# Kernel tuning notes

Measured on AMD Instinct MI355X. Metric: run time of the kernel, lower is better.

## Reference

```python
import jax, jax.numpy as jnp
import numpy as np

N = 50000
E = 800000
IN_CH = 512
OUT_CH = 64
ITERATIONS = 3  # adjacency power order; iterations-1 spmm steps


def setup_inputs() -> dict:
    key = jax.random.key(0)
    k1, k2, k3, k4, k5 = jax.random.split(key, 5)
    adj_indices = jax.random.randint(k1, (2, E), 0, N, dtype=jnp.int32)
    adj_values = jax.random.uniform(k2, (E,), dtype=jnp.float32)
    features = jax.random.normal(k3, (N, IN_CH), dtype=jnp.float32)
    # xavier-uniform init bounds
    bw = float(np.sqrt(6.0 / (IN_CH + OUT_CH)))
    weight = jax.random.uniform(k4, (IN_CH, OUT_CH), minval=-bw, maxval=bw, dtype=jnp.float32)
    bb = float(np.sqrt(6.0 / (1 + OUT_CH)))
    bias = jax.random.uniform(k5, (1, OUT_CH), minval=-bb, maxval=bb, dtype=jnp.float32)
    return {"adj_indices": adj_indices, "adj_values": adj_values,
            "features": features, "weight": weight, "bias": bias}


def reference(adj_indices, adj_values, features, weight, bias):
    # dense projection: [N, in] @ [in, out] -> [N, out]
    x = features @ weight
    # dropout is identity in eval mode (training=False)
    row, col = adj_indices[0], adj_indices[1]
    # (iterations - 1) sparse-dense matmuls: x <- A @ x
    for _ in range(ITERATIONS - 1):
        gathered = adj_values[:, None] * x[col]          # [E, out]
        x = jax.ops.segment_sum(gathered, row, num_segments=N)
    return x + bias
```

## Files before the change

### kernel.cpp

```cpp
#include <hip/hip_runtime.h>
#include <hip/hip_bf16.h>
#include <hip/hip_fp16.h>

#define NN 50000
#define INCH 512
#define OUTCH 64
#define NTILES 3125
#define MAXD 48
#define GB 782
#define SB 512

typedef __attribute__((ext_vector_type(8))) short short8;
typedef __attribute__((ext_vector_type(4))) float floatx4;

__device__ __forceinline__ unsigned packbf2(float a, float b) {
    __hip_bfloat162 h = __float22bfloat162_rn(make_float2(a, b));
    unsigned r;
    __builtin_memcpy(&r, &h, 4);
    return r;
}
__device__ __forceinline__ unsigned short f2bf(float f) {
    unsigned u = __float_as_uint(f);
    return (unsigned short)((u + 0x7FFFu + ((u >> 16) & 1u)) >> 16);
}
__device__ __forceinline__ float bf2f(unsigned short u) {
    return __uint_as_float(((unsigned)u) << 16);
}

__global__ __launch_bounds__(256) void prep_kernel(const float* __restrict__ W,
                                                   unsigned short* __restrict__ Wbf,
                                                   int* __restrict__ deg) {
    const int i = blockIdx.x * 256 + threadIdx.x;
    if (i < NN / 4)
        *reinterpret_cast<uint4*>(deg + i * 4) = uint4{0u, 0u, 0u, 0u};
    if (i < INCH * OUTCH) {
        const int k = i >> 6;
        const int n = i & 63;
        Wbf[n * INCH + k] = f2bf(W[i]);
    }
}

__global__ __launch_bounds__(256, 4) void fused_gemm_scatter(
        const float* __restrict__ A, const unsigned short* __restrict__ Wbf,
        unsigned short* __restrict__ C,
        const int* __restrict__ rows, const int* __restrict__ cols,
        const float* __restrict__ vals, int* __restrict__ deg,
        unsigned* __restrict__ ell, int E_) {
    __shared__ unsigned short ldsT[4][16 * 64];
    const int t = threadIdx.x;

    if (blockIdx.x >= GB) {
        for (int e = (blockIdx.x - GB) * 256 + t; e < E_; e += SB * 256) {
            const int r = __builtin_nontemporal_load(rows + e);
            const int c = __builtin_nontemporal_load(cols + e);
            const float v = __builtin_nontemporal_load(vals + e);
            const int slot = atomicAdd(&deg[r], 1);
            const unsigned short hv = __half_as_ushort(__float2half(v));
            if (slot < MAXD)
                ell[(size_t)r * MAXD + slot] = (unsigned)c | ((unsigned)hv << 16);
        }
        return;
    }

    const int lane = t & 63;
    const int wave = t >> 6;
    const int tile = blockIdx.x * 4 + wave;
    if (tile >= NTILES) return;
    const int rbase = tile * 16;
    const int frow = lane & 15;
    const int quad = lane >> 4;
    const float* Ap = A + (size_t)(rbase + frow) * INCH + quad * 8;
    const unsigned short* Bp = Wbf + frow * INCH + quad * 8;

    floatx4 acc[4] = {floatx4{0,0,0,0}, floatx4{0,0,0,0}, floatx4{0,0,0,0}, floatx4{0,0,0,0}};

#pragma unroll
    for (int c = 0; c < 16; ++c) {
        const floatx4 a0 = __builtin_nontemporal_load((const floatx4*)(Ap + c * 32));
        const floatx4 a1 = __builtin_nontemporal_load((const floatx4*)(Ap + c * 32 + 4));
        short8 bfr[4];
#pragma unroll
        for (int f = 0; f < 4; ++f)
            bfr[f] = *(const short8*)(Bp + (size_t)f * 16 * INCH + c * 32);
        uint4 au;
        au.x = packbf2(a0[0], a0[1]);
        au.y = packbf2(a0[2], a0[3]);
        au.z = packbf2(a1[0], a1[1]);
        au.w = packbf2(a1[2], a1[3]);
        const short8 af = *(const short8*)&au;
#pragma unroll
        for (int f = 0; f < 4; ++f)
            acc[f] = __builtin_amdgcn_mfma_f32_16x16x32_bf16(af, bfr[f], acc[f], 0, 0, 0);
    }

    unsigned short* myT = ldsT[wave];
#pragma unroll
    for (int f = 0; f < 4; ++f)
#pragma unroll
        for (int reg = 0; reg < 4; ++reg)
            myT[(quad * 4 + reg) * 64 + f * 16 + frow] = f2bf(acc[f][reg]);
    unsigned short* Cw = C + (size_t)rbase * OUTCH;
#pragma unroll
    for (int it = 0; it < 2; ++it) {
        const short8 v = *(const short8*)&myT[it * 512 + lane * 8];
        __builtin_nontemporal_store(v, (short8*)(Cw + it * 512 + lane * 8));
    }
}

template <bool LAST>
__global__ __launch_bounds__(256) void spmm_ell(const int* __restrict__ deg,
                                                const unsigned* __restrict__ ell,
                                                const unsigned short* __restrict__ xin,
                                                void* __restrict__ xout_,
                                                const float* __restrict__ bias) {
    const int b = blockIdx.x;
    const int xcd = b & 7;
    const int half = xcd >> 2;
    const int rowgrp = (b >> 3) * 4 + (xcd & 3);
    const int t = threadIdx.x;
    const int lane = t & 63;
    const int eslot = lane >> 2;
    const int cg = lane & 3;
    const int row = rowgrp * 4 + (t >> 6);
    int d = __builtin_nontemporal_load(deg + row);
    d = d < MAXD ? d : MAXD;
    const unsigned* ebase = ell + (size_t)row * MAXD;

    unsigned p0 = __builtin_nontemporal_load(ebase + eslot);
    unsigned p1 = __builtin_nontemporal_load(ebase + eslot + 16);
    unsigned p2 = __builtin_nontemporal_load(ebase + eslot + 32);
    if (eslot >= d)      p0 = 0u;
    if (eslot + 16 >= d) p1 = 0u;
    if (eslot + 32 >= d) p2 = 0u;

    const unsigned short* xh = xin + half * 32 + cg * 8;
    float acc[8] = {0.f, 0.f, 0.f, 0.f, 0.f, 0.f, 0.f, 0.f};

    auto gath = [&](unsigned P) {
        const short8 xv = *(const short8*)(xh + (size_t)(P & 0xFFFFu) * OUTCH);
        const float v = __half2float(__ushort_as_half((unsigned short)(P >> 16)));
#pragma unroll
        for (int j = 0; j < 8; ++j)
            acc[j] = fmaf(v, bf2f((unsigned short)xv[j]), acc[j]);
    };
    if (d > 0)  gath(p0);
    if (d > 16) gath(p1);
    if (d > 32) gath(p2);

#pragma unroll
    for (int j = 0; j < 8; ++j) {
        acc[j] += __shfl_xor(acc[j], 4, 64);
        acc[j] += __shfl_xor(acc[j], 8, 64);
        acc[j] += __shfl_xor(acc[j], 16, 64);
        acc[j] += __shfl_xor(acc[j], 32, 64);
    }

    if (eslot == 0) {
        const int chb = half * 32 + cg * 8;
        if (LAST) {
            float* op = (float*)xout_ + (size_t)row * OUTCH + chb;
            const floatx4 b0 = *(const floatx4*)(bias + chb);
            const floatx4 b1 = *(const floatx4*)(bias + chb + 4);
            floatx4 o0, o1;
            o0[0] = acc[0] + b0[0]; o0[1] = acc[1] + b0[1];
            o0[2] = acc[2] + b0[2]; o0[3] = acc[3] + b0[3];
            o1[0] = acc[4] + b1[0]; o1[1] = acc[5] + b1[1];
            o1[2] = acc[6] + b1[2]; o1[3] = acc[7] + b1[3];
            __builtin_nontemporal_store(o0, (floatx4*)op);
            __builtin_nontemporal_store(o1, (floatx4*)(op + 4));
        } else {
            unsigned short* op = (unsigned short*)xout_ + (size_t)row * OUTCH + chb;
            short8 o;
#pragma unroll
            for (int j = 0; j < 8; ++j) o[j] = (short)f2bf(acc[j]);
            __builtin_nontemporal_store(o, (short8*)op);
        }
    }
}

extern "C" void kernel_launch(void* const* d_in, const int* in_sizes, int n_in,
                              void* d_out, int out_size, void* d_ws, size_t ws_size,
                              hipStream_t stream) {
    const int*   adj   = (const int*)d_in[0];
    const float* avals = (const float*)d_in[1];
    const float* feat  = (const float*)d_in[2];
    const float* W     = (const float*)d_in[3];
    const float* bias  = (const float*)d_in[4];
    float* out = (float*)d_out;

    const int E_ = in_sizes[1];
    const int* rows = adj;
    const int* cols = adj + E_;

    unsigned short* x0  = (unsigned short*)d_ws;
    unsigned short* x1  = x0 + (size_t)NN * OUTCH;
    unsigned short* Wbf = x1 + (size_t)NN * OUTCH;
    unsigned* ell = (unsigned*)(Wbf + (size_t)OUTCH * INCH);
    int* deg = (int*)(ell + (size_t)NN * MAXD);

    prep_kernel<<<128, 256, 0, stream>>>(W, Wbf, deg);

    fused_gemm_scatter<<<GB + SB, 256, 0, stream>>>(feat, Wbf, x0, rows, cols, avals,
                                                    deg, ell, E_);

    spmm_ell<false><<<25000, 256, 0, stream>>>(deg, ell, x0, x1, nullptr);
    spmm_ell<true><<<25000, 256, 0, stream>>>(deg, ell, x1, out, bias);
}
```

Before: 288.9 us.

## Split scatter into row-range passes and SpMM into per-half-channel launches

Separates the fused GEMM+scatter kernel into a standalone GEMM and four scatter passes, each handling a quarter of the destination rows, so atomics and ELL writes hit a smaller working set that fits in cache. The SpMM is split into two launches per iteration, each covering 32 channels, which replaces the XCD-aware block swizzle. Intermediate stores become regular rather than nontemporal so x1 stays cached for the next step. The cost is re-reading the row array four times, losing the overlap between GEMM and scatter, and more kernel launches.

```diff
diff --git a/kernel.cpp b/kernel.cpp
--- a/kernel.cpp
+++ b/kernel.cpp
@@ -8,7 +8,8 @@
 #define NTILES 3125
 #define MAXD 48
 #define GB 782
-#define SB 512
+#define SCB 512
+#define ROWS_PER_PASS 12500
 
 typedef __attribute__((ext_vector_type(8))) short short8;
 typedef __attribute__((ext_vector_type(4))) float floatx4;
@@ -40,28 +41,11 @@
     }
 }
 
-__global__ __launch_bounds__(256, 4) void fused_gemm_scatter(
+__global__ __launch_bounds__(256, 4) void gemm_kernel(
         const float* __restrict__ A, const unsigned short* __restrict__ Wbf,
-        unsigned short* __restrict__ C,
-        const int* __restrict__ rows, const int* __restrict__ cols,
-        const float* __restrict__ vals, int* __restrict__ deg,
-        unsigned* __restrict__ ell, int E_) {
+        unsigned short* __restrict__ C) {
     __shared__ unsigned short ldsT[4][16 * 64];
     const int t = threadIdx.x;
-
-    if (blockIdx.x >= GB) {
-        for (int e = (blockIdx.x - GB) * 256 + t; e < E_; e += SB * 256) {
-            const int r = __builtin_nontemporal_load(rows + e);
-            const int c = __builtin_nontemporal_load(cols + e);
-            const float v = __builtin_nontemporal_load(vals + e);
-            const int slot = atomicAdd(&deg[r], 1);
-            const unsigned short hv = __half_as_ushort(__float2half(v));
-            if (slot < MAXD)
-                ell[(size_t)r * MAXD + slot] = (unsigned)c | ((unsigned)hv << 16);
-        }
-        return;
-    }
-
     const int lane = t & 63;
     const int wave = t >> 6;
     const int tile = blockIdx.x * 4 + wave;
@@ -107,22 +91,37 @@
     }
 }
 
+__global__ __launch_bounds__(256) void scatter_pass(
+        const int* __restrict__ rows, const int* __restrict__ cols,
+        const float* __restrict__ vals, int* __restrict__ deg,
+        unsigned* __restrict__ ell, int E_, int rowlo) {
+    for (int e = blockIdx.x * 256 + threadIdx.x; e < E_; e += SCB * 256) {
+        const int r = __builtin_nontemporal_load(rows + e);
+        if ((unsigned)(r - rowlo) < (unsigned)ROWS_PER_PASS) {
+            const int c = __builtin_nontemporal_load(cols + e);
+            const float v = __builtin_nontemporal_load(vals + e);
+            const int slot = atomicAdd(&deg[r], 1);
+            if (slot < MAXD) {
+                const unsigned short hv = __half_as_ushort(__float2half(v));
+                ell[(size_t)r * MAXD + slot] = (unsigned)c | ((unsigned)hv << 16);
+            }
+        }
+    }
+}
+
 template <bool LAST>
-__global__ __launch_bounds__(256) void spmm_ell(const int* __restrict__ deg,
-                                                const unsigned* __restrict__ ell,
-                                                const unsigned short* __restrict__ xin,
-                                                void* __restrict__ xout_,
-                                                const float* __restrict__ bias) {
-    const int b = blockIdx.x;
-    const int xcd = b & 7;
-    const int half = xcd >> 2;
-    const int rowgrp = (b >> 3) * 4 + (xcd & 3);
+__global__ __launch_bounds__(256) void spmm_half(const int* __restrict__ deg,
+                                                 const unsigned* __restrict__ ell,
+                                                 const unsigned short* __restrict__ xin,
+                                                 void* __restrict__ xout_,
+                                                 const float* __restrict__ bias,
+                                                 int chbase) {
     const int t = threadIdx.x;
     const int lane = t & 63;
     const int eslot = lane >> 2;
     const int cg = lane & 3;
-    const int row = rowgrp * 4 + (t >> 6);
-    int d = __builtin_nontemporal_load(deg + row);
+    const int row = blockIdx.x * 4 + (t >> 6);
+    int d = deg[row];
     d = d < MAXD ? d : MAXD;
     const unsigned* ebase = ell + (size_t)row * MAXD;
 
@@ -133,7 +132,7 @@
     if (eslot + 16 >= d) p1 = 0u;
     if (eslot + 32 >= d) p2 = 0u;
 
-    const unsigned short* xh = xin + half * 32 + cg * 8;
+    const unsigned short* xh = xin + chbase + cg * 8;
     float acc[8] = {0.f, 0.f, 0.f, 0.f, 0.f, 0.f, 0.f, 0.f};
 
     auto gath = [&](unsigned P) {
@@ -156,7 +155,7 @@
     }
 
     if (eslot == 0) {
-        const int chb = half * 32 + cg * 8;
+        const int chb = chbase + cg * 8;
         if (LAST) {
             float* op = (float*)xout_ + (size_t)row * OUTCH + chb;
             const floatx4 b0 = *(const floatx4*)(bias + chb);
@@ -173,7 +172,7 @@
             short8 o;
 #pragma unroll
             for (int j = 0; j < 8; ++j) o[j] = (short)f2bf(acc[j]);
-            __builtin_nontemporal_store(o, (short8*)op);
+            *(short8*)op = o;
         }
     }
 }
@@ -200,9 +199,14 @@
 
     prep_kernel<<<128, 256, 0, stream>>>(W, Wbf, deg);
 
-    fused_gemm_scatter<<<GB + SB, 256, 0, stream>>>(feat, Wbf, x0, rows, cols, avals,
-                                                    deg, ell, E_);
-
-    spmm_ell<false><<<25000, 256, 0, stream>>>(deg, ell, x0, x1, nullptr);
-    spmm_ell<true><<<25000, 256, 0, stream>>>(deg, ell, x1, out, bias);
-}
+    gemm_kernel<<<GB, 256, 0, stream>>>(feat, Wbf, x0);
+
+    for (int p = 0; p < 4; ++p)
+        scatter_pass<<<SCB, 256, 0, stream>>>(rows, cols, avals, deg, ell, E_,
+                                              p * ROWS_PER_PASS);
+
+    spmm_half<false><<<NN / 4, 256, 0, stream>>>(deg, ell, x0, x1, nullptr, 0);
+    spmm_half<false><<<NN / 4, 256, 0, stream>>>(deg, ell, x0, x1, nullptr, 32);
+    spmm_half<true><<<NN / 4, 256, 0, stream>>>(deg, ell, x1, out, bias, 0);
+    spmm_half<true><<<NN / 4, 256, 0, stream>>>(deg, ell, x1, out, bias, 32);
+}
```

After: 328.9 us. 1.14x slower.

## Split ELL adjacency by column half and run SpMM in two phases

Applied to the files above, without the earlier changes.

Edges are bucketed by whether the column index falls in the lower or upper half of the nodes, giving two ELL structures with 32 slots each. Each SpMM step becomes two kernels: the first gathers from the lower half of x into an fp32 partial buffer, and the second gathers from the upper half and adds the partial. The aim is to keep each phase's gather working set (half of x) resident in cache and to drop the XCD-based channel split. In exchange it adds two extra launches and an fp32 partial round-trip through memory, and each half now drops edges beyond 32 per row.

```diff
diff --git a/kernel.cpp b/kernel.cpp
--- a/kernel.cpp
+++ b/kernel.cpp
@@ -6,12 +6,14 @@
 #define INCH 512
 #define OUTCH 64
 #define NTILES 3125
-#define MAXD 48
+#define MAXDH 32
+#define COLSPLIT 25000
 #define GB 782
 #define SB 512
 
 typedef __attribute__((ext_vector_type(8))) short short8;
 typedef __attribute__((ext_vector_type(4))) float floatx4;
+typedef __attribute__((ext_vector_type(4))) unsigned short ushortx4;
 
 __device__ __forceinline__ unsigned packbf2(float a, float b) {
     __hip_bfloat162 h = __float22bfloat162_rn(make_float2(a, b));
@@ -29,10 +31,10 @@
 
 __global__ __launch_bounds__(256) void prep_kernel(const float* __restrict__ W,
                                                    unsigned short* __restrict__ Wbf,
-                                                   int* __restrict__ deg) {
+                                                   int* __restrict__ degs) {
     const int i = blockIdx.x * 256 + threadIdx.x;
-    if (i < NN / 4)
-        *reinterpret_cast<uint4*>(deg + i * 4) = uint4{0u, 0u, 0u, 0u};
+    if (i < (2 * NN) / 4)
+        *reinterpret_cast<uint4*>(degs + i * 4) = uint4{0u, 0u, 0u, 0u};
     if (i < INCH * OUTCH) {
         const int k = i >> 6;
         const int n = i & 63;
@@ -44,8 +46,9 @@
         const float* __restrict__ A, const unsigned short* __restrict__ Wbf,
         unsigned short* __restrict__ C,
         const int* __restrict__ rows, const int* __restrict__ cols,
-        const float* __restrict__ vals, int* __restrict__ deg,
-        unsigned* __restrict__ ell, int E_) {
+        const float* __restrict__ vals, int* __restrict__ deg_lo,
+        int* __restrict__ deg_hi, unsigned* __restrict__ ell_lo,
+        unsigned* __restrict__ ell_hi, int E_) {
     __shared__ unsigned short ldsT[4][16 * 64];
     const int t = threadIdx.x;
 
@@ -54,10 +57,14 @@
             const int r = __builtin_nontemporal_load(rows + e);
             const int c = __builtin_nontemporal_load(cols + e);
             const float v = __builtin_nontemporal_load(vals + e);
-            const int slot = atomicAdd(&deg[r], 1);
-            const unsigned short hv = __half_as_ushort(__float2half(v));
-            if (slot < MAXD)
-                ell[(size_t)r * MAXD + slot] = (unsigned)c | ((unsigned)hv << 16);
+            const int hi = (c >= COLSPLIT);
+            int* dg = hi ? deg_hi : deg_lo;
+            unsigned* el = hi ? ell_hi : ell_lo;
+            const int slot = atomicAdd(&dg[r], 1);
+            if (slot < MAXDH) {
+                const unsigned short hv = __half_as_ushort(__float2half(v));
+                el[(size_t)r * MAXDH + slot] = (unsigned)c | ((unsigned)hv << 16);
+            }
         }
         return;
     }
@@ -107,73 +114,66 @@
     }
 }
 
-template <bool LAST>
-__global__ __launch_bounds__(256) void spmm_ell(const int* __restrict__ deg,
-                                                const unsigned* __restrict__ ell,
-                                                const unsigned short* __restrict__ xin,
-                                                void* __restrict__ xout_,
-                                                const float* __restrict__ bias) {
-    const int b = blockIdx.x;
-    const int xcd = b & 7;
-    const int half = xcd >> 2;
-    const int rowgrp = (b >> 3) * 4 + (xcd & 3);
+template <int MODE>
+__global__ __launch_bounds__(256) void spmm_phase(
+        const int* __restrict__ degs, const unsigned* __restrict__ ells,
+        const unsigned short* __restrict__ xin, float* __restrict__ partial,
+        void* __restrict__ xout_, const float* __restrict__ bias) {
     const int t = threadIdx.x;
     const int lane = t & 63;
-    const int eslot = lane >> 2;
-    const int cg = lane & 3;
-    const int row = rowgrp * 4 + (t >> 6);
-    int d = __builtin_nontemporal_load(deg + row);
-    d = d < MAXD ? d : MAXD;
-    const unsigned* ebase = ell + (size_t)row * MAXD;
-
-    unsigned p0 = __builtin_nontemporal_load(ebase + eslot);
-    unsigned p1 = __builtin_nontemporal_load(ebase + eslot + 16);
-    unsigned p2 = __builtin_nontemporal_load(ebase + eslot + 32);
-    if (eslot >= d)      p0 = 0u;
-    if (eslot + 16 >= d) p1 = 0u;
-    if (eslot + 32 >= d) p2 = 0u;
-
-    const unsigned short* xh = xin + half * 32 + cg * 8;
-    float acc[8] = {0.f, 0.f, 0.f, 0.f, 0.f, 0.f, 0.f, 0.f};
-
-    auto gath = [&](unsigned P) {
-        const short8 xv = *(const short8*)(xh + (size_t)(P & 0xFFFFu) * OUTCH);
-        const float v = __half2float(__ushort_as_half((unsigned short)(P >> 16)));
-#pragma unroll
-        for (int j = 0; j < 8; ++j)
-            acc[j] = fmaf(v, bf2f((unsigned short)xv[j]), acc[j]);
-    };
-    if (d > 0)  gath(p0);
-    if (d > 16) gath(p1);
-    if (d > 32) gath(p2);
-
+    const int eslot = lane >> 4;
+    const int cl = lane & 15;
+    const int row = blockIdx.x * 4 + (t >> 6);
+    int d = degs[row];
+    d = d < MAXDH ? d : MAXDH;
+    const unsigned* eb = ells + (size_t)row * MAXDH;
+
+    unsigned p[8];
+#pragma unroll
+    for (int j = 0; j < 8; ++j)
+        p[j] = __builtin_nontemporal_load(eb + eslot + 4 * j);
+#pragma unroll
+    for (int j = 0; j < 8; ++j)
+        if (eslot + 4 * j >= d) p[j] = 0u;
+
+    float a0 = 0.f, a1 = 0.f, a2 = 0.f, a3 = 0.f;
 #pragma unroll
     for (int j = 0; j < 8; ++j) {
-        acc[j] += __shfl_xor(acc[j], 4, 64);
-        acc[j] += __shfl_xor(acc[j], 8, 64);
-        acc[j] += __shfl_xor(acc[j], 16, 64);
-        acc[j] += __shfl_xor(acc[j], 32, 64);
-    }
+        if (d > 4 * j) {
+            const unsigned P = p[j];
+            const ushortx4 xv = *(const ushortx4*)(xin + (size_t)(P & 0xFFFFu) * OUTCH + cl * 4);
+            const float v = __half2float(__ushort_as_half((unsigned short)(P >> 16)));
+            a0 = fmaf(v, bf2f(xv[0]), a0);
+            a1 = fmaf(v, bf2f(xv[1]), a1);
+            a2 = fmaf(v, bf2f(xv[2]), a2);
+            a3 = fmaf(v, bf2f(xv[3]), a3);
+        }
+    }
+
+    a0 += __shfl_xor(a0, 16, 64); a1 += __shfl_xor(a1, 16, 64);
+    a2 += __shfl_xor(a2, 16, 64); a3 += __shfl_xor(a3, 16, 64);
+    a0 += __shfl_xor(a0, 32, 64); a1 += __shfl_xor(a1, 32, 64);
+    a2 += __shfl_xor(a2, 32, 64); a3 += __shfl_xor(a3, 32, 64);
 
     if (eslot == 0) {
-        const int chb = half * 32 + cg * 8;
-        if (LAST) {
-            float* op = (float*)xout_ + (size_t)row * OUTCH + chb;
-            const floatx4 b0 = *(const floatx4*)(bias + chb);
-            const floatx4 b1 = *(const floatx4*)(bias + chb + 4);
-            floatx4 o0, o1;
-            o0[0] = acc[0] + b0[0]; o0[1] = acc[1] + b0[1];
-            o0[2] = acc[2] + b0[2]; o0[3] = acc[3] + b0[3];
-            o1[0] = acc[4] + b1[0]; o1[1] = acc[5] + b1[1];
-            o1[2] = acc[6] + b1[2]; o1[3] = acc[7] + b1[3];
-            __builtin_nontemporal_store(o0, (floatx4*)op);
-            __builtin_nontemporal_store(o1, (floatx4*)(op + 4));
+        const int chb = cl * 4;
+        if (MODE == 0) {
+            floatx4 o = {a0, a1, a2, a3};
+            __builtin_nontemporal_store(o, (floatx4*)(partial + (size_t)row * OUTCH + chb));
         } else {
-            unsigned short* op = (unsigned short*)xout_ + (size_t)row * OUTCH + chb;
-            short8 o;
-#pragma unroll
-            for (int j = 0; j < 8; ++j) o[j] = (short)f2bf(acc[j]);
-            __builtin_nontemporal_store(o, (short8*)op);
+            const floatx4 pp = __builtin_nontemporal_load(
+                (const floatx4*)(partial + (size_t)row * OUTCH + chb));
+            a0 += pp[0]; a1 += pp[1]; a2 += pp[2]; a3 += pp[3];
+            if (MODE == 1) {
+                ushortx4 o = {f2bf(a0), f2bf(a1), f2bf(a2), f2bf(a3)};
+                __builtin_nontemporal_store(
+                    o, (ushortx4*)((unsigned short*)xout_ + (size_t)row * OUTCH + chb));
+            } else {
+                const floatx4 bv = *(const floatx4*)(bias + chb);
+                floatx4 o = {a0 + bv[0], a1 + bv[1], a2 + bv[2], a3 + bv[3]};
+                __builtin_nontemporal_store(
+                    o, (floatx4*)((float*)xout_ + (size_t)row * OUTCH + chb));
+            }
         }
     }
 }
@@ -195,14 +195,20 @@
     unsigned short* x0  = (unsigned short*)d_ws;
     unsigned short* x1  = x0 + (size_t)NN * OUTCH;
     unsigned short* Wbf = x1 + (size_t)NN * OUTCH;
-    unsigned* ell = (unsigned*)(Wbf + (size_t)OUTCH * INCH);
-    int* deg = (int*)(ell + (size_t)NN * MAXD);
-
-    prep_kernel<<<128, 256, 0, stream>>>(W, Wbf, deg);
+    unsigned* ell_lo = (unsigned*)(Wbf + (size_t)OUTCH * INCH);
+    unsigned* ell_hi = ell_lo + (size_t)NN * MAXDH;
+    int* deg_lo = (int*)(ell_hi + (size_t)NN * MAXDH);
+    int* deg_hi = deg_lo + NN;
+    float* partial = (float*)(deg_hi + NN);
+
+    prep_kernel<<<128, 256, 0, stream>>>(W, Wbf, deg_lo);
 
     fused_gemm_scatter<<<GB + SB, 256, 0, stream>>>(feat, Wbf, x0, rows, cols, avals,
-                                                    deg, ell, E_);
-
-    spmm_ell<false><<<25000, 256, 0, stream>>>(deg, ell, x0, x1, nullptr);
-    spmm_ell<true><<<25000, 256, 0, stream>>>(deg, ell, x1, out, bias);
-}
+                                                    deg_lo, deg_hi, ell_lo, ell_hi, E_);
+
+    spmm_phase<0><<<NN / 4, 256, 0, stream>>>(deg_lo, ell_lo, x0, partial, nullptr, nullptr);
+    spmm_phase<1><<<NN / 4, 256, 0, stream>>>(deg_hi, ell_hi, x0, partial, x1, nullptr);
+
+    spmm_phase<0><<<NN / 4, 256, 0, stream>>>(deg_lo, ell_lo, x1, partial, nullptr, nullptr);
+    spmm_phase<2><<<NN / 4, 256, 0, stream>>>(deg_hi, ell_hi, x1, partial, out, bias);
+}
```

Result: no change. 291.6 us (+0.9%).

## Process all 64 channels per wave in SpMM instead of splitting halves across XCDs

Applied to the files above, without the earlier changes.

The SpMM kernel now has each wave handle a full row across all 64 output channels, with 8 edge slots times 8 channel groups, instead of splitting the channel halves across XCD-mapped blocks. This halves the grid size and the number of ELL index reads per row, and drops one shuffle-reduction stage, but it gives up the XCD-local L2 partitioning of the feature matrix. It also makes the ELL scatter writes nontemporal and moves the half conversion inside the bounds check.

```diff
diff --git a/kernel.cpp b/kernel.cpp
--- a/kernel.cpp
+++ b/kernel.cpp
@@ -55,9 +55,11 @@
             const int c = __builtin_nontemporal_load(cols + e);
             const float v = __builtin_nontemporal_load(vals + e);
             const int slot = atomicAdd(&deg[r], 1);
-            const unsigned short hv = __half_as_ushort(__float2half(v));
-            if (slot < MAXD)
-                ell[(size_t)r * MAXD + slot] = (unsigned)c | ((unsigned)hv << 16);
+            if (slot < MAXD) {
+                const unsigned short hv = __half_as_ushort(__float2half(v));
+                __builtin_nontemporal_store((unsigned)c | ((unsigned)hv << 16),
+                                            &ell[(size_t)r * MAXD + slot]);
+            }
         }
         return;
     }
@@ -108,55 +110,52 @@
 }
 
 template <bool LAST>
-__global__ __launch_bounds__(256) void spmm_ell(const int* __restrict__ deg,
-                                                const unsigned* __restrict__ ell,
-                                                const unsigned short* __restrict__ xin,
-                                                void* __restrict__ xout_,
-                                                const float* __restrict__ bias) {
-    const int b = blockIdx.x;
-    const int xcd = b & 7;
-    const int half = xcd >> 2;
-    const int rowgrp = (b >> 3) * 4 + (xcd & 3);
+__global__ __launch_bounds__(256) void spmm_full(const int* __restrict__ deg,
+                                                 const unsigned* __restrict__ ell,
+                                                 const unsigned short* __restrict__ xin,
+                                                 void* __restrict__ xout_,
+                                                 const float* __restrict__ bias) {
     const int t = threadIdx.x;
     const int lane = t & 63;
-    const int eslot = lane >> 2;
-    const int cg = lane & 3;
-    const int row = rowgrp * 4 + (t >> 6);
-    int d = __builtin_nontemporal_load(deg + row);
+    const int eslot = lane >> 3;
+    const int cg = lane & 7;
+    const int row = blockIdx.x * 4 + (t >> 6);
+    int d = deg[row];
     d = d < MAXD ? d : MAXD;
-    const unsigned* ebase = ell + (size_t)row * MAXD;
-
-    unsigned p0 = __builtin_nontemporal_load(ebase + eslot);
-    unsigned p1 = __builtin_nontemporal_load(ebase + eslot + 16);
-    unsigned p2 = __builtin_nontemporal_load(ebase + eslot + 32);
-    if (eslot >= d)      p0 = 0u;
-    if (eslot + 16 >= d) p1 = 0u;
-    if (eslot + 32 >= d) p2 = 0u;
-
-    const unsigned short* xh = xin + half * 32 + cg * 8;
+    const unsigned* eb = ell + (size_t)row * MAXD;
+
+    unsigned p[6];
+#pragma unroll
+    for (int j = 0; j < 6; ++j)
+        p[j] = __builtin_nontemporal_load(eb + eslot + 8 * j);
+#pragma unroll
+    for (int j = 0; j < 6; ++j)
+        if (eslot + 8 * j >= d) p[j] = 0u;
+
+    const unsigned short* xh = xin + cg * 8;
     float acc[8] = {0.f, 0.f, 0.f, 0.f, 0.f, 0.f, 0.f, 0.f};
 
-    auto gath = [&](unsigned P) {
-        const short8 xv = *(const short8*)(xh + (size_t)(P & 0xFFFFu) * OUTCH);
-        const float v = __half2float(__ushort_as_half((unsigned short)(P >> 16)));
-#pragma unroll
-        for (int j = 0; j < 8; ++j)
-            acc[j] = fmaf(v, bf2f((unsigned short)xv[j]), acc[j]);
-    };
-    if (d > 0)  gath(p0);
-    if (d > 16) gath(p1);
-    if (d > 32) gath(p2);
-
-#pragma unroll
-    for (int j = 0; j < 8; ++j) {
-        acc[j] += __shfl_xor(acc[j], 4, 64);
-        acc[j] += __shfl_xor(acc[j], 8, 64);
-        acc[j] += __shfl_xor(acc[j], 16, 64);
-        acc[j] += __shfl_xor(acc[j], 32, 64);
+#pragma unroll
+    for (int j = 0; j < 6; ++j) {
+        if (d > 8 * j) {
+            const unsigned P = p[j];
+            const short8 xv = *(const short8*)(xh + (size_t)(P & 0xFFFFu) * OUTCH);
+            const float v = __half2float(__ushort_as_half((unsigned short)(P >> 16)));
+#pragma unroll
+            for (int k = 0; k < 8; ++k)
+                acc[k] = fmaf(v, bf2f((unsigned short)xv[k]), acc[k]);
+        }
+    }
+
+#pragma unroll
+    for (int k = 0; k < 8; ++k) {
+        acc[k] += __shfl_xor(acc[k], 8, 64);
+        acc[k] += __shfl_xor(acc[k], 16, 64);
+        acc[k] += __shfl_xor(acc[k], 32, 64);
     }
 
     if (eslot == 0) {
-        const int chb = half * 32 + cg * 8;
+        const int chb = cg * 8;
         if (LAST) {
             float* op = (float*)xout_ + (size_t)row * OUTCH + chb;
             const floatx4 b0 = *(const floatx4*)(bias + chb);
@@ -172,7 +171,7 @@
             unsigned short* op = (unsigned short*)xout_ + (size_t)row * OUTCH + chb;
             short8 o;
 #pragma unroll
-            for (int j = 0; j < 8; ++j) o[j] = (short)f2bf(acc[j]);
+            for (int k = 0; k < 8; ++k) o[k] = (short)f2bf(acc[k]);
             __builtin_nontemporal_store(o, (short8*)op);
         }
     }
@@ -203,6 +202,6 @@
     fused_gemm_scatter<<<GB + SB, 256, 0, stream>>>(feat, Wbf, x0, rows, cols, avals,
                                                     deg, ell, E_);
 
-    spmm_ell<false><<<25000, 256, 0, stream>>>(deg, ell, x0, x1, nullptr);
-    spmm_ell<true><<<25000, 256, 0, stream>>>(deg, ell, x1, out, bias);
-}
+    spmm_full<false><<<NN / 4, 256, 0, stream>>>(deg, ell, x0, x1, nullptr);
+    spmm_full<true><<<NN / 4, 256, 0, stream>>>(deg, ell, x1, out, bias);
+}
```

New measurement: 253.4 us. 1.14x faster.
